# Optimization experiments

Measured on AMD Instinct MI355X. Metric: run time of the kernel, lower is better.

Reference implementation:

```python
import jax, jax.numpy as jnp
import numpy as np

NUM_TRUE = 8
NUM_NULL = 2
NUM_EXPERTS = NUM_TRUE + NUM_NULL
TOP_K = 2


def setup_inputs() -> dict:
    key = jax.random.key(0)
    k0, k1, k2 = jax.random.split(key, 3)
    B, S, D = 4, 2048, 1024
    inputs = jax.random.normal(k0, (B, S, D), dtype=jnp.float32)
    gate_w = jax.random.normal(k1, (NUM_EXPERTS, D), dtype=jnp.float32) * 0.02
    gate_b = jnp.zeros((NUM_EXPERTS,), dtype=jnp.float32)
    # expert_w stored as [E, D_in, D_out] so expert i computes x @ expert_w[i] + expert_b[i]
    expert_w = jax.random.normal(k2, (NUM_TRUE, D, D), dtype=jnp.float32) * 0.02
    expert_b = jnp.zeros((NUM_TRUE, D), dtype=jnp.float32)
    return {"inputs": inputs, "gate_w": gate_w, "gate_b": gate_b,
            "expert_w": expert_w, "expert_b": expert_b}


def reference(inputs, gate_w, gate_b, expert_w, expert_b):
    D = inputs.shape[-1]
    x = inputs.reshape(-1, D)                       # [T, D]
    gate_logits = x @ gate_w.T + gate_b             # [T, E]
    gate_probs = jax.nn.softmax(gate_logits, axis=-1)
    weights, selected = jax.lax.top_k(gate_probs, TOP_K)  # [T, K]
    true_mask = selected < NUM_TRUE                 # null experts contribute nothing
    true_weights = weights * true_mask
    denom = true_weights.sum(axis=-1, keepdims=True)
    denom = jnp.where(denom > 0, denom, jnp.ones_like(denom))
    norm_w = (true_weights / denom).astype(x.dtype)  # [T, K]
    # per-(token, true-expert) combine weight; zero for unselected experts
    one_hot = jax.nn.one_hot(selected, NUM_EXPERTS, dtype=norm_w.dtype)  # [T, K, E]
    combine_w = jnp.einsum('tk,tke->te', norm_w, one_hot)[:, :NUM_TRUE]  # [T, E_true]
    # dense expert evaluation, then weighted combine (zero weights cancel
    # exactly as the gather/scatter loop in the torch code)
    expert_out = jnp.einsum('td,edh->teh', x, expert_w) + expert_b[None, :, :]  # [T, E_true, D]
    out = jnp.einsum('te,teh->th', combine_w, expert_out)  # [T, D]
    return out.reshape(inputs.shape[:-1] + (out.shape[-1],))
```

## Files before the change

### kernel.cpp

```cpp
#include <hip/hip_runtime.h>
#include <hip/hip_bf16.h>
#include <stdint.h>

#define T_TOKENS 8192
#define D_DIM    1024
#define NE       10
#define NT       8
#define SEG      2048

typedef unsigned short u16;
typedef __attribute__((ext_vector_type(8))) __bf16 bf16x8;
typedef __attribute__((ext_vector_type(4))) float  f32x4;
typedef __attribute__((ext_vector_type(8))) unsigned short u16x8;
typedef __attribute__((ext_vector_type(4))) unsigned short u16x4;

static __device__ __forceinline__ u16 f32_to_bf16(float f) {
  union { float f; uint32_t u; } v; v.f = f;
  uint32_t u = v.u;
  return (u16)((u + 0x7fffu + ((u >> 16) & 1u)) >> 16);
}
static __device__ __forceinline__ float bf16_to_f32(u16 u) {
  union { uint32_t u; float f; } v; v.u = ((uint32_t)u) << 16; return v.f;
}

static __device__ __forceinline__ void async_load16(const u16* g, u16* l) {
  __builtin_amdgcn_global_load_lds(
      (const __attribute__((address_space(1))) void*)(const void*)g,
      (__attribute__((address_space(3))) void*)(void*)l, 16, 0, 0);
}

union PrepShared {
  struct { float gws[NE * D_DIM]; float gbs[NE]; int se[32]; float swt[32]; } g;
  struct { float tile[64][65]; } t;
};

__global__ __launch_bounds__(256) void prep_kernel(
    const float* __restrict__ x, const float* __restrict__ gw,
    const float* __restrict__ gb, const float* __restrict__ W,
    u16* __restrict__ xb, u16* __restrict__ wT,
    int* __restrict__ cnt, int* __restrict__ tokList,
    int* __restrict__ revIdx, float* __restrict__ revW) {
  __shared__ PrepShared sh;
  int tid = threadIdx.x;

  if (blockIdx.x >= 512) {
    int tb = blockIdx.x - 512;
    int e  = tb >> 8;
    int rem = tb & 255;
    int k0 = (rem >> 4) * 64;
    int n0 = (rem & 15) * 64;
    int c  = tid & 63;
    int r0 = tid >> 6;
    const float* We = W + ((size_t)e << 20);
#pragma unroll
    for (int rr = 0; rr < 16; ++rr) {
      int r = rr * 4 + r0;
      sh.t.tile[c][r] = We[(size_t)(k0 + r) * 1024 + n0 + c];
    }
    __syncthreads();
    u16* wTe = wT + ((size_t)e << 20);
#pragma unroll
    for (int rr = 0; rr < 16; ++rr) {
      int n = rr * 4 + r0;
      wTe[(size_t)(n0 + n) * 1024 + k0 + c] = f32_to_bf16(sh.t.tile[n][c]);
    }
    return;
  }

  {
    const f32x4* g4 = (const f32x4*)gw;
    f32x4* s4 = (f32x4*)sh.g.gws;
    for (int i = tid; i < NE * D_DIM / 4; i += 256) s4[i] = g4[i];
  }
  if (tid < NE) sh.g.gbs[tid] = gb[tid];
  __syncthreads();
  int lane = tid & 63;
  int wv   = tid >> 6;
  const f32x4* gws4 = (const f32x4*)sh.g.gws;
  for (int it = 0; it < 4; ++it) {
    int slot = wv * 4 + it;
    int t = blockIdx.x * 16 + slot;
    const f32x4* xr4 = (const f32x4*)(x + (size_t)t * D_DIM);
    f32x4 xv[4];
#pragma unroll
    for (int jj = 0; jj < 4; ++jj) xv[jj] = xr4[lane + 64 * jj];
    u16x4* xbr = (u16x4*)(xb + (size_t)t * D_DIM);
#pragma unroll
    for (int jj = 0; jj < 4; ++jj) {
      u16x4 pk;
#pragma unroll
      for (int k = 0; k < 4; ++k) pk[k] = f32_to_bf16(xv[jj][k]);
      xbr[lane + 64 * jj] = pk;
    }
    float logit[NE];
#pragma unroll
    for (int e = 0; e < NE; ++e) {
      float a = 0.f;
#pragma unroll
      for (int jj = 0; jj < 4; ++jj) {
        f32x4 gv = gws4[e * 256 + lane + 64 * jj];
#pragma unroll
        for (int k = 0; k < 4; ++k) a = fmaf(xv[jj][k], gv[k], a);
      }
#pragma unroll
      for (int off = 32; off >= 1; off >>= 1) a += __shfl_xor(a, off);
      logit[e] = a + sh.g.gbs[e];
    }
    float mx = logit[0];
#pragma unroll
    for (int e = 1; e < NE; ++e) mx = fmaxf(mx, logit[e]);
    float p[NE]; float s = 0.f;
#pragma unroll
    for (int e = 0; e < NE; ++e) { p[e] = expf(logit[e] - mx); s += p[e]; }
    int e0 = 0; float b0 = p[0];
#pragma unroll
    for (int e = 1; e < NE; ++e) if (p[e] > b0) { b0 = p[e]; e0 = e; }
    int e1 = -1; float b1 = -1.f;
#pragma unroll
    for (int e = 0; e < NE; ++e) if (e != e0 && p[e] > b1) { b1 = p[e]; e1 = e; }
    float w0 = b0 / s, w1 = b1 / s;
    float tw0 = (e0 < NT) ? w0 : 0.f;
    float tw1 = (e1 < NT) ? w1 : 0.f;
    float denom = tw0 + tw1;
    float nw0 = 0.f, nw1 = 0.f;
    if (denom > 0.f) { nw0 = tw0 / denom; nw1 = tw1 / denom; }
    if (lane == 0) {
      sh.g.se[slot * 2]     = (e0 < NT) ? e0 : -1;  sh.g.swt[slot * 2]     = nw0;
      sh.g.se[slot * 2 + 1] = (e1 < NT) ? e1 : -1;  sh.g.swt[slot * 2 + 1] = nw1;
      if (e0 >= NT) { revIdx[t * 2]     = -1; revW[t * 2]     = 0.f; }
      if (e1 >= NT) { revIdx[t * 2 + 1] = -1; revW[t * 2 + 1] = 0.f; }
    }
  }
  __syncthreads();
  if (tid < NT) {
    int e = tid, c = 0;
    for (int i = 0; i < 32; ++i) c += (sh.g.se[i] == e);
    if (c > 0) {
      int base = atomicAdd(&cnt[e * 32], c);
      int j = 0;
      for (int i = 0; i < 32; ++i) {
        if (sh.g.se[i] == e) {
          int tt  = blockIdx.x * 16 + (i >> 1);
          int pos = base + j;
          tokList[e * SEG + pos]   = tt;
          revIdx[tt * 2 + (i & 1)] = e * SEG + pos;
          revW[tt * 2 + (i & 1)]   = sh.g.swt[i];
          ++j;
        }
      }
    }
  }
}

__global__ __launch_bounds__(256) void moe_gemm(
    const u16* __restrict__ xb, const u16* __restrict__ wT,
    const int* __restrict__ cnt, const int* __restrict__ tokList,
    const float* __restrict__ eb, u16* __restrict__ ybuf) {
  int e  = blockIdx.x;
  int c  = cnt[e * 32];
  int m0 = blockIdx.z * 128;
  if (m0 >= c) return;
  int n0 = blockIdx.y * 128;
  __shared__ __align__(16) u16 As[3][128 * 32];
  __shared__ __align__(16) u16 Bs[3][128 * 32];
  __shared__ int tokS[128];
  int tid = threadIdx.x;
  if (tid < 128) {
    int gm = m0 + tid;
    tokS[tid] = (gm < c) ? tokList[e * SEG + gm] : tokList[e * SEG];
  }
  __syncthreads();
  int lane = tid & 63;
  int wv   = tid >> 6;
  int rl  = lane >> 2;
  int kcp = lane & 3;
  int kcd = kcp ^ (rl & 3);
  int rowL0 = wv * 32 + rl, rowL1 = rowL0 + 16;
  const u16* gA0 = xb + (size_t)tokS[rowL0] * 1024 + kcd * 8;
  const u16* gA1 = xb + (size_t)tokS[rowL1] * 1024 + kcd * 8;
  const u16* wTe = wT + ((size_t)e << 20);
  const u16* gB0 = wTe + (size_t)(n0 + rowL0) * 1024 + kcd * 8;
  const u16* gB1 = wTe + (size_t)(n0 + rowL1) * 1024 + kcd * 8;
  int ldsA0 = (wv * 32) * 32, ldsA1 = (wv * 32 + 16) * 32;

  int wm = wv >> 1, wn = wv & 1;
  int lrow = lane & 15;
  int q    = lane >> 4;
  int sw   = (q ^ (lrow & 3)) * 8;
  f32x4 acc[4][4];
#pragma unroll
  for (int i = 0; i < 4; ++i)
#pragma unroll
    for (int j = 0; j < 4; ++j) acc[i][j] = (f32x4){0.f, 0.f, 0.f, 0.f};

#pragma unroll
  for (int p = 0; p < 2; ++p) {
    int ko = p * 32;
    async_load16(gA0 + ko, As[p] + ldsA0);
    async_load16(gA1 + ko, As[p] + ldsA1);
    async_load16(gB0 + ko, Bs[p] + ldsA0);
    async_load16(gB1 + ko, Bs[p] + ldsA1);
  }

  int cur = 0;
  for (int kt = 0; kt < 32; ++kt) {
    asm volatile("s_barrier" ::: "memory");
    if (kt < 30) {
      int st = cur - 1; if (st < 0) st += 3;
      int ko = (kt + 2) * 32;
      async_load16(gA0 + ko, As[st] + ldsA0);
      async_load16(gA1 + ko, As[st] + ldsA1);
      async_load16(gB0 + ko, Bs[st] + ldsA0);
      async_load16(gB1 + ko, Bs[st] + ldsA1);
      asm volatile("s_waitcnt vmcnt(8)" ::: "memory");
    } else if (kt == 30) {
      asm volatile("s_waitcnt vmcnt(4)" ::: "memory");
    } else {
      asm volatile("s_waitcnt vmcnt(0)" ::: "memory");
    }
    asm volatile("s_barrier" ::: "memory");
    bf16x8 af[4], bfr[4];
#pragma unroll
    for (int mt = 0; mt < 4; ++mt)
      af[mt] = *(const bf16x8*)(As[cur] + (wm * 64 + mt * 16 + lrow) * 32 + sw);
#pragma unroll
    for (int nt = 0; nt < 4; ++nt)
      bfr[nt] = *(const bf16x8*)(Bs[cur] + (wn * 64 + nt * 16 + lrow) * 32 + sw);
#pragma unroll
    for (int mt = 0; mt < 4; ++mt)
#pragma unroll
      for (int nt = 0; nt < 4; ++nt)
        acc[mt][nt] = __builtin_amdgcn_mfma_f32_16x16x32_bf16(
            af[mt], bfr[nt], acc[mt][nt], 0, 0, 0);
    ++cur; if (cur == 3) cur = 0;
  }
  int rq = lane >> 4;
  float bias[4];
#pragma unroll
  for (int nt = 0; nt < 4; ++nt)
    bias[nt] = eb[e * 1024 + n0 + wn * 64 + nt * 16 + lrow];
  u16* yb = ybuf + ((size_t)(e * SEG + m0)) * 1024 + n0 + wn * 64 + lrow;
#pragma unroll
  for (int mt = 0; mt < 4; ++mt) {
#pragma unroll
    for (int r = 0; r < 4; ++r) {
      int ml = wm * 64 + mt * 16 + rq * 4 + r;
      u16* row = yb + (size_t)ml * 1024;
#pragma unroll
      for (int nt = 0; nt < 4; ++nt)
        row[nt * 16] = f32_to_bf16(acc[mt][nt][r] + bias[nt]);
    }
  }
}

__global__ __launch_bounds__(256) void combine_kernel(
    const u16* __restrict__ ybuf, const int* __restrict__ revIdx,
    const float* __restrict__ revW, float* __restrict__ out) {
  int tid = threadIdx.x, lane = tid & 63, wv = tid >> 6;
  for (int it = 0; it < 4; ++it) {
    int t  = blockIdx.x * 16 + wv * 4 + it;
    int i0 = revIdx[t * 2], i1 = revIdx[t * 2 + 1];
    float w0 = revW[t * 2], w1 = revW[t * 2 + 1];
    float o[16];
#pragma unroll
    for (int k = 0; k < 16; ++k) o[k] = 0.f;
    if (i0 >= 0) {
      const u16x8* y = (const u16x8*)(ybuf + (size_t)i0 * 1024);
#pragma unroll
      for (int jj = 0; jj < 2; ++jj) {
        u16x8 v = y[lane + 64 * jj];
#pragma unroll
        for (int k = 0; k < 8; ++k) o[jj * 8 + k] += w0 * bf16_to_f32(v[k]);
      }
    }
    if (i1 >= 0) {
      const u16x8* y = (const u16x8*)(ybuf + (size_t)i1 * 1024);
#pragma unroll
      for (int jj = 0; jj < 2; ++jj) {
        u16x8 v = y[lane + 64 * jj];
#pragma unroll
        for (int k = 0; k < 8; ++k) o[jj * 8 + k] += w1 * bf16_to_f32(v[k]);
      }
    }
    f32x4* o4 = (f32x4*)(out + (size_t)t * 1024);
#pragma unroll
    for (int jj = 0; jj < 2; ++jj)
#pragma unroll
      for (int h = 0; h < 2; ++h) {
        f32x4 vv = {o[jj * 8 + h * 4], o[jj * 8 + h * 4 + 1],
                    o[jj * 8 + h * 4 + 2], o[jj * 8 + h * 4 + 3]};
        o4[2 * (lane + 64 * jj) + h] = vv;
      }
  }
}

extern "C" void kernel_launch(void* const* d_in, const int* in_sizes, int n_in,
                              void* d_out, int out_size, void* d_ws, size_t ws_size,
                              hipStream_t stream) {
  const float* x  = (const float*)d_in[0];
  const float* gw = (const float*)d_in[1];
  const float* gb = (const float*)d_in[2];
  const float* ew = (const float*)d_in[3];
  const float* eb = (const float*)d_in[4];
  float* out = (float*)d_out;
  char* ws = (char*)d_ws;
  int*   cnt     = (int*)ws;
  int*   tokList = (int*)(ws + 4096);
  int*   revIdx  = (int*)(ws + 4096 + 65536);
  float* revW    = (float*)(ws + 4096 + 131072);
  u16*   xb      = (u16*)(ws + 200704);
  u16*   wT      = (u16*)(ws + 200704 + 16777216);
  u16*   ybuf    = (u16*)(ws + 200704 + 33554432);

  hipMemsetAsync(cnt, 0, 4096, stream);
  prep_kernel<<<2560, 256, 0, stream>>>(x, gw, gb, ew, xb, wT, cnt, tokList,
                                        revIdx, revW);
  moe_gemm<<<dim3(8, 8, 16), 256, 0, stream>>>(xb, wT, cnt, tokList, eb, ybuf);
  combine_kernel<<<512, 256, 0, stream>>>(ybuf, revIdx, revW, out);
}
```

Before: 178.5 us.

## Fuse combine into GEMM epilogue via weighted atomic adds to output

Removes the separate combine kernel and the bf16 intermediate expert-output buffer. The GEMM epilogue now scales each row by its routing weight and atomically adds it into the fp32 output, which extra blocks in the prep kernel zero first. The LDS swizzle pattern is also changed to XOR with the row index shifted right by one, presumably to reduce bank conflicts. In exchange the output is written with scattered fp32 atomics rather than coalesced vector stores, and the summation order becomes nondeterministic.

Result: slower. 207.6 us (+16.3%).

```diff
diff --git a/kernel.cpp b/kernel.cpp
--- a/kernel.cpp
+++ b/kernel.cpp
@@ -19,9 +19,6 @@
   uint32_t u = v.u;
   return (u16)((u + 0x7fffu + ((u >> 16) & 1u)) >> 16);
 }
-static __device__ __forceinline__ float bf16_to_f32(u16 u) {
-  union { uint32_t u; float f; } v; v.u = ((uint32_t)u) << 16; return v.f;
-}
 
 static __device__ __forceinline__ void async_load16(const u16* g, u16* l) {
   __builtin_amdgcn_global_load_lds(
@@ -39,10 +36,17 @@
     const float* __restrict__ gb, const float* __restrict__ W,
     u16* __restrict__ xb, u16* __restrict__ wT,
     int* __restrict__ cnt, int* __restrict__ tokList,
-    int* __restrict__ revIdx, float* __restrict__ revW) {
+    float* __restrict__ wList, float* __restrict__ out) {
   __shared__ PrepShared sh;
   int tid = threadIdx.x;
 
+  if (blockIdx.x >= 2560) {
+    int zr = blockIdx.x - 2560;
+    f32x4* o4 = (f32x4*)out + (size_t)zr * 8192;
+    f32x4 z = {0.f, 0.f, 0.f, 0.f};
+    for (int i = tid; i < 8192; i += 256) o4[i] = z;
+    return;
+  }
   if (blockIdx.x >= 512) {
     int tb = blockIdx.x - 512;
     int e  = tb >> 8;
@@ -127,24 +131,21 @@
     if (lane == 0) {
       sh.g.se[slot * 2]     = (e0 < NT) ? e0 : -1;  sh.g.swt[slot * 2]     = nw0;
       sh.g.se[slot * 2 + 1] = (e1 < NT) ? e1 : -1;  sh.g.swt[slot * 2 + 1] = nw1;
-      if (e0 >= NT) { revIdx[t * 2]     = -1; revW[t * 2]     = 0.f; }
-      if (e1 >= NT) { revIdx[t * 2 + 1] = -1; revW[t * 2 + 1] = 0.f; }
     }
   }
   __syncthreads();
   if (tid < NT) {
-    int e = tid, c = 0;
-    for (int i = 0; i < 32; ++i) c += (sh.g.se[i] == e);
-    if (c > 0) {
-      int base = atomicAdd(&cnt[e * 32], c);
+    int e = tid, cc = 0;
+    for (int i = 0; i < 32; ++i) cc += (sh.g.se[i] == e);
+    if (cc > 0) {
+      int base = atomicAdd(&cnt[e * 32], cc);
       int j = 0;
       for (int i = 0; i < 32; ++i) {
         if (sh.g.se[i] == e) {
           int tt  = blockIdx.x * 16 + (i >> 1);
           int pos = base + j;
-          tokList[e * SEG + pos]   = tt;
-          revIdx[tt * 2 + (i & 1)] = e * SEG + pos;
-          revW[tt * 2 + (i & 1)]   = sh.g.swt[i];
+          tokList[e * SEG + pos] = tt;
+          wList[e * SEG + pos]   = sh.g.swt[i];
           ++j;
         }
       }
@@ -155,7 +156,8 @@
 __global__ __launch_bounds__(256) void moe_gemm(
     const u16* __restrict__ xb, const u16* __restrict__ wT,
     const int* __restrict__ cnt, const int* __restrict__ tokList,
-    const float* __restrict__ eb, u16* __restrict__ ybuf) {
+    const float* __restrict__ wList, const float* __restrict__ eb,
+    float* __restrict__ out) {
   int e  = blockIdx.x;
   int c  = cnt[e * 32];
   int m0 = blockIdx.z * 128;
@@ -163,18 +165,21 @@
   int n0 = blockIdx.y * 128;
   __shared__ __align__(16) u16 As[3][128 * 32];
   __shared__ __align__(16) u16 Bs[3][128 * 32];
-  __shared__ int tokS[128];
+  __shared__ int   tokS[128];
+  __shared__ float wS[128];
   int tid = threadIdx.x;
   if (tid < 128) {
     int gm = m0 + tid;
-    tokS[tid] = (gm < c) ? tokList[e * SEG + gm] : tokList[e * SEG];
+    int valid = gm < c;
+    tokS[tid] = valid ? tokList[e * SEG + gm] : tokList[e * SEG];
+    wS[tid]   = valid ? wList[e * SEG + gm] : 0.f;
   }
   __syncthreads();
   int lane = tid & 63;
   int wv   = tid >> 6;
   int rl  = lane >> 2;
   int kcp = lane & 3;
-  int kcd = kcp ^ (rl & 3);
+  int kcd = kcp ^ ((rl >> 1) & 3);
   int rowL0 = wv * 32 + rl, rowL1 = rowL0 + 16;
   const u16* gA0 = xb + (size_t)tokS[rowL0] * 1024 + kcd * 8;
   const u16* gA1 = xb + (size_t)tokS[rowL1] * 1024 + kcd * 8;
@@ -186,7 +191,7 @@
   int wm = wv >> 1, wn = wv & 1;
   int lrow = lane & 15;
   int q    = lane >> 4;
-  int sw   = (q ^ (lrow & 3)) * 8;
+  int sw   = (q ^ ((lrow >> 1) & 3)) * 8;
   f32x4 acc[4][4];
 #pragma unroll
   for (int i = 0; i < 4; ++i)
@@ -239,58 +244,19 @@
 #pragma unroll
   for (int nt = 0; nt < 4; ++nt)
     bias[nt] = eb[e * 1024 + n0 + wn * 64 + nt * 16 + lrow];
-  u16* yb = ybuf + ((size_t)(e * SEG + m0)) * 1024 + n0 + wn * 64 + lrow;
 #pragma unroll
   for (int mt = 0; mt < 4; ++mt) {
 #pragma unroll
     for (int r = 0; r < 4; ++r) {
       int ml = wm * 64 + mt * 16 + rq * 4 + r;
-      u16* row = yb + (size_t)ml * 1024;
-#pragma unroll
-      for (int nt = 0; nt < 4; ++nt)
-        row[nt * 16] = f32_to_bf16(acc[mt][nt][r] + bias[nt]);
-    }
-  }
-}
-
-__global__ __launch_bounds__(256) void combine_kernel(
-    const u16* __restrict__ ybuf, const int* __restrict__ revIdx,
-    const float* __restrict__ revW, float* __restrict__ out) {
-  int tid = threadIdx.x, lane = tid & 63, wv = tid >> 6;
-  for (int it = 0; it < 4; ++it) {
-    int t  = blockIdx.x * 16 + wv * 4 + it;
-    int i0 = revIdx[t * 2], i1 = revIdx[t * 2 + 1];
-    float w0 = revW[t * 2], w1 = revW[t * 2 + 1];
-    float o[16];
-#pragma unroll
-    for (int k = 0; k < 16; ++k) o[k] = 0.f;
-    if (i0 >= 0) {
-      const u16x8* y = (const u16x8*)(ybuf + (size_t)i0 * 1024);
-#pragma unroll
-      for (int jj = 0; jj < 2; ++jj) {
-        u16x8 v = y[lane + 64 * jj];
-#pragma unroll
-        for (int k = 0; k < 8; ++k) o[jj * 8 + k] += w0 * bf16_to_f32(v[k]);
+      float w = wS[ml];
+      if (w != 0.f) {
+        float* orow = out + (size_t)tokS[ml] * 1024 + n0 + wn * 64 + lrow;
+#pragma unroll
+        for (int nt = 0; nt < 4; ++nt)
+          atomicAdd(&orow[nt * 16], w * (acc[mt][nt][r] + bias[nt]));
       }
     }
-    if (i1 >= 0) {
-      const u16x8* y = (const u16x8*)(ybuf + (size_t)i1 * 1024);
-#pragma unroll
-      for (int jj = 0; jj < 2; ++jj) {
-        u16x8 v = y[lane + 64 * jj];
-#pragma unroll
-        for (int k = 0; k < 8; ++k) o[jj * 8 + k] += w1 * bf16_to_f32(v[k]);
-      }
-    }
-    f32x4* o4 = (f32x4*)(out + (size_t)t * 1024);
-#pragma unroll
-    for (int jj = 0; jj < 2; ++jj)
-#pragma unroll
-      for (int h = 0; h < 2; ++h) {
-        f32x4 vv = {o[jj * 8 + h * 4], o[jj * 8 + h * 4 + 1],
-                    o[jj * 8 + h * 4 + 2], o[jj * 8 + h * 4 + 3]};
-        o4[2 * (lane + 64 * jj) + h] = vv;
-      }
   }
 }
 
@@ -306,15 +272,13 @@
   char* ws = (char*)d_ws;
   int*   cnt     = (int*)ws;
   int*   tokList = (int*)(ws + 4096);
-  int*   revIdx  = (int*)(ws + 4096 + 65536);
-  float* revW    = (float*)(ws + 4096 + 131072);
+  float* wList   = (float*)(ws + 4096 + 65536);
   u16*   xb      = (u16*)(ws + 200704);
   u16*   wT      = (u16*)(ws + 200704 + 16777216);
-  u16*   ybuf    = (u16*)(ws + 200704 + 33554432);
 
   hipMemsetAsync(cnt, 0, 4096, stream);
-  prep_kernel<<<2560, 256, 0, stream>>>(x, gw, gb, ew, xb, wT, cnt, tokList,
-                                        revIdx, revW);
-  moe_gemm<<<dim3(8, 8, 16), 256, 0, stream>>>(xb, wT, cnt, tokList, eb, ybuf);
-  combine_kernel<<<512, 256, 0, stream>>>(ybuf, revIdx, revW, out);
-}
+  prep_kernel<<<2816, 256, 0, stream>>>(x, gw, gb, ew, xb, wT, cnt, tokList,
+                                        wList, out);
+  moe_gemm<<<dim3(8, 8, 16), 256, 0, stream>>>(xb, wT, cnt, tokList, wList,
+                                               eb, out);
+}
```
